# Performance work log

Hardware: AMD Instinct MI355X
Metric: run time of the kernel (lower is better)

## Reference

```python
import jax, jax.numpy as jnp
import numpy as np

H = 1024      # hidden_size
NH = 16       # num_attention_heads
DK = H // NH  # head dim
C = 1024      # cyclic_size


def setup_inputs() -> dict:
    key = jax.random.key(0)
    ks = jax.random.split(key, 13)
    B, S = 2, 2048
    s = 1.0 / np.sqrt(H)
    inp = {
        "q": jax.random.normal(ks[0], (B, S, H), jnp.float32),
        "k": jax.random.normal(ks[1], (B, S, H), jnp.float32),
        "v": jax.random.normal(ks[2], (B, S, H), jnp.float32),
        "Wq": jax.random.normal(ks[3], (H, H), jnp.float32) * s,
        "bq": jnp.zeros((H,), jnp.float32),
        "Wk": jax.random.normal(ks[4], (H, H), jnp.float32) * s,
        "bk": jnp.zeros((H,), jnp.float32),
        "Wv": jax.random.normal(ks[5], (H, H), jnp.float32) * s,
        "bv": jnp.zeros((H,), jnp.float32),
        "Wo": jax.random.normal(ks[6], (H, H), jnp.float32) * s,
        "bo": jnp.zeros((H,), jnp.float32),
        "Wc": jax.random.normal(ks[7], (H, C), jnp.float32) * s,
        "bc": jnp.zeros((C,), jnp.float32),
    }
    return inp


def _split_heads(x):
    B, S, _ = x.shape
    return x.reshape(B, S, NH, DK).transpose(0, 2, 1, 3)  # [B,NH,S,DK]


def reference(q, k, v, Wq, bq, Wk, bk, Wv, bv, Wo, bo, Wc, bc):
    Q = _split_heads(q @ Wq + bq)
    K = _split_heads(k @ Wk + bk)
    V = _split_heads(v @ Wv + bv)
    # unfused SDPA: full [B,NH,S,S] scores, as in the original module
    scores = jnp.einsum("bhqd,bhkd->bhqk", Q, K) / jnp.sqrt(jnp.float32(DK))
    probs = jax.nn.softmax(scores, axis=-1)
    attn = jnp.einsum("bhqk,bhkd->bhqd", probs, V)  # [B,NH,S,DK]
    B, _, S, _ = attn.shape
    merged = attn.transpose(0, 2, 1, 3).reshape(B, S, H)
    h = merged @ Wo + bo
    c = merged @ Wc + bc
    return (c, h)
```

## Files before the change

### kernel.cpp

```cpp
#include <hip/hip_runtime.h>
#include <stdint.h>

typedef unsigned short u16;
typedef short bf16x8 __attribute__((ext_vector_type(8)));
typedef short bf16x4 __attribute__((ext_vector_type(4)));
typedef float f32x4 __attribute__((ext_vector_type(4)));

#define MB (1u<<20)
#define CL2 0.18033688f

static __device__ __forceinline__ u16 f2bf(float x){
  union { float f; unsigned u; } v; v.f = x;
  return (u16)((v.u + 0x7FFFu + ((v.u >> 16) & 1u)) >> 16);
}

static __device__ __forceinline__ void gld_lds16(const void* g, void* l){
  __builtin_amdgcn_global_load_lds((const __attribute__((address_space(1))) unsigned int*)g,
                                   (__attribute__((address_space(3))) unsigned int*)l, 16, 0, 0);
}

static __device__ __forceinline__ int pack_bf16(float a, float b){
  unsigned ua = __float_as_uint(a) + 0x8000u;
  unsigned ub = __float_as_uint(b) + 0x8000u;
  return (int)__builtin_amdgcn_perm(ub, ua, 0x07060302u);
}

__global__ void convx(const float* __restrict__ q, const float* __restrict__ k, const float* __restrict__ v,
                      u16* __restrict__ qb, u16* __restrict__ kb, u16* __restrict__ vb){
  const float* s = blockIdx.z==0 ? q : (blockIdx.z==1 ? k : v);
  u16* d = blockIdx.z==0 ? qb : (blockIdx.z==1 ? kb : vb);
  int i = (blockIdx.x*256 + threadIdx.x)*4;
  float4 f = *(const float4*)(s + i);
  ushort4 o; o.x=f2bf(f.x); o.y=f2bf(f.y); o.z=f2bf(f.z); o.w=f2bf(f.w);
  *(ushort4*)(d + i) = o;
}

__global__ void convw(const float* W0,const float* W1,const float* W2,const float* W3,const float* W4,
                      u16* T0,u16* T1,u16* T2,u16* T3,u16* T4){
  const float* W = blockIdx.z==0?W0:blockIdx.z==1?W1:blockIdx.z==2?W2:blockIdx.z==3?W3:W4;
  u16* T = blockIdx.z==0?T0:blockIdx.z==1?T1:blockIdx.z==2?T2:blockIdx.z==3?T3:T4;
  __shared__ u16 t[64][65];
  int k0 = blockIdx.x*64, n0 = blockIdx.y*64;
  for (int i=0;i<16;i++){
    int idx = i*256 + threadIdx.x;
    int r = idx >> 6, c = idx & 63;
    t[r][c] = f2bf(W[(size_t)(k0+r)*1024 + n0 + c]);
  }
  __syncthreads();
  for (int i=0;i<2;i++){
    int idx = i*256 + threadIdx.x;
    int nl = idx >> 3, kc = idx & 7;
    bf16x8 o;
    #pragma unroll
    for (int j=0;j<8;j++) o[j] = (short)t[kc*8+j][nl];
    *(bf16x8*)(T + (size_t)(n0+nl)*1024 + k0 + kc*8) = o;
  }
}

template<int MODE>
static __device__ __forceinline__ void gemm_bt_dev(u16* __restrict__ As, u16* __restrict__ Bs,
                                                   const u16* __restrict__ A, const u16* __restrict__ Bt,
                                                   const float* __restrict__ bias, void* __restrict__ Cout){
  const int tid = threadIdx.x, lane = tid & 63, w = tid >> 6;
  const int wm = w >> 1, wn = w & 1, quad = lane >> 4, lr = lane & 15;
  const int fid = blockIdx.y * 8 + blockIdx.x;
  const int o   = (fid & 7) * 32 + (fid >> 3);
  const int n0  = (o & 7) * 128, m0 = (o >> 3) * 128;
  f32x4 acc[4][4] = {};
  const u16* Ab = A + (size_t)m0*1024;
  const u16* Bb = Bt + (size_t)n0*1024;
  const int srow_base = w*8 + (lane >> 3);
  const int sg = lane & 7;
  for (int k0 = 0; k0 < 1024; k0 += 64){
    #pragma unroll
    for (int j = 0; j < 4; ++j){
      int row = j*32 + srow_base;
      int g = sg ^ (row & 7);
      gld_lds16(Ab + (size_t)row*1024 + k0 + g*8, As + (j*32 + w*8)*64);
      gld_lds16(Bb + (size_t)row*1024 + k0 + g*8, Bs + (j*32 + w*8)*64);
    }
    __syncthreads();
    #pragma unroll
    for (int kk = 0; kk < 2; ++kk){
      bf16x8 af[4], bfr[4];
      #pragma unroll
      for (int i=0;i<4;i++){
        int ra = wm*64 + i*16 + lr;
        af[i]  = *(const bf16x8*)(As + ra*64 + (((kk*4+quad) ^ (ra & 7)))*8);
        int rb = wn*64 + i*16 + lr;
        bfr[i] = *(const bf16x8*)(Bs + rb*64 + (((kk*4+quad) ^ (rb & 7)))*8);
      }
      #pragma unroll
      for (int mi=0;mi<4;mi++)
        #pragma unroll
        for (int ni=0;ni<4;ni++)
          acc[mi][ni] = __builtin_amdgcn_mfma_f32_16x16x32_bf16(af[mi], bfr[ni], acc[mi][ni], 0, 0, 0);
    }
    __syncthreads();
  }
  #pragma unroll
  for (int mi=0;mi<4;mi++){
    int row = m0 + wm*64 + mi*16 + quad*4;
    #pragma unroll
    for (int ni=0;ni<4;ni++){
      int col = n0 + wn*64 + ni*16 + lr;
      float bb = bias[col];
      #pragma unroll
      for (int rg=0; rg<4; rg++){
        float vv = acc[mi][ni][rg] + bb;
        int r = row + rg;
        if (MODE == 0){
          ((u16*)Cout)[(size_t)r*1024 + col] = f2bf(vv);
        } else if (MODE == 4){
          ((u16*)Cout)[(size_t)r*1024 + col] = f2bf(vv * CL2);
        } else if (MODE == 1){
          ((float*)Cout)[(size_t)r*1024 + col] = vv;
        } else if (MODE == 2){
          int b2 = r >> 11, s = r & 2047, kb2 = s >> 7, kvl = s & 127;
          int hh = col >> 6, hg = (col & 63) >> 3, hl = col & 7;
          ((u16*)Cout)[((size_t)(b2*16+hh)*16 + kb2)*8192 + hg*1024 + kvl*8 + hl] = f2bf(vv);
        } else {
          int b2 = r >> 11, s = r & 2047, kb2 = s >> 7, kvl = s & 127;
          int mt2v = kvl >> 5, gv = (kvl >> 2) & 3, jv = ((kvl >> 4) & 1)*4 + (kvl & 3);
          int hh = col >> 6, dd = col & 63;
          ((u16*)Cout)[((size_t)(b2*16+hh)*16 + kb2)*8192 + (size_t)(mt2v*4+gv)*512 + dd*8 + jv] = f2bf(vv);
        }
      }
    }
  }
}

__global__ void qkv_gemm(const u16* qb,const u16* kb,const u16* vb,
                         const u16* Wqt,const u16* Wkt,const u16* Wvt,
                         const float* bq,const float* bk,const float* bv,
                         u16* Qb,u16* Kr,u16* Vr){
  __shared__ u16 As[128*64];
  __shared__ u16 Bs[128*64];
  if (blockIdx.z == 0)      gemm_bt_dev<4>(As, Bs, qb, Wqt, bq, Qb);
  else if (blockIdx.z == 1) gemm_bt_dev<2>(As, Bs, kb, Wkt, bk, Kr);
  else                      gemm_bt_dev<3>(As, Bs, vb, Wvt, bv, Vr);
}

__global__ void out_gemm(const u16* Mg, const u16* Wct, const u16* Wot,
                         const float* bc, const float* bo, float* out){
  __shared__ u16 As[128*64];
  __shared__ u16 Bs[128*64];
  const u16* B = blockIdx.z==0? Wct : Wot;
  const float* bias = blockIdx.z==0? bc : bo;
  float* C = out + (blockIdx.z==0? 0 : 4194304);
  gemm_bt_dev<1>(As, Bs, Mg, B, bias, C);
}

__global__ __launch_bounds__(256,2) void attn(const u16* __restrict__ Qb, const u16* __restrict__ Kr,
                                              const u16* __restrict__ Vr, u16* __restrict__ Mg){
  __shared__ u16 Ks[2][8192];
  __shared__ u16 Vs[2][8192];
  const int fid = blockIdx.y * 16 + blockIdx.x;
  const int o   = (fid & 7) * 64 + (fid >> 3);
  const int qt = o & 15, bh = o >> 4, b = bh >> 4, h = bh & 15;
  const int tid = threadIdx.x, lane = tid & 63, w = tid >> 6;
  const int quad = lane >> 4, lr = lane & 15;
  const int q0 = qt*128 + w*32;

  bf16x8 aq[2][2];
  #pragma unroll
  for (int t=0;t<2;t++)
    #pragma unroll
    for (int ks=0;ks<2;ks++)
      aq[t][ks] = *(const bf16x8*)(Qb + (size_t)(b*2048 + q0 + t*16 + lr)*1024 + h*64 + ks*32 + quad*8);

  f32x4 acco[2][4] = {};
  f32x4 accl[2] = {};
  const bf16x8 ones8 = {(short)0x3F80,(short)0x3F80,(short)0x3F80,(short)0x3F80,
                        (short)0x3F80,(short)0x3F80,(short)0x3F80,(short)0x3F80};

  const u16* Krb = Kr + (size_t)bh*131072;
  const u16* Vrb = Vr + (size_t)bh*131072;

  #pragma unroll
  for (int j=0;j<4;j++){
    gld_lds16(Krb + j*2048 + tid*8, &Ks[0][j*2048 + w*512]);
    gld_lds16(Vrb + j*2048 + tid*8, &Vs[0][j*2048 + w*512]);
  }

  for (int kb = 0; kb < 16; kb++){
    __syncthreads();
    const int cur = kb & 1;
    if (kb < 15){
      const u16* kg = Krb + (size_t)(kb+1)*8192;
      const u16* vg = Vrb + (size_t)(kb+1)*8192;
      #pragma unroll
      for (int j=0;j<4;j++){
        gld_lds16(kg + j*2048 + tid*8, &Ks[cur^1][j*2048 + w*512]);
        gld_lds16(vg + j*2048 + tid*8, &Vs[cur^1][j*2048 + w*512]);
      }
    }
    const u16* Ksc = Ks[cur];
    const u16* Vsc = Vs[cur];

    #pragma unroll
    for (int mt2=0;mt2<4;mt2++){
      f32x4 ae0 = {}, ae1 = {}, ao0 = {}, ao1 = {};
      {
        bf16x8 kf0 = *(const bf16x8*)(Ksc + (0*4+quad)*1024 + ((2*mt2)*16+lr)*8);
        bf16x8 kf1 = *(const bf16x8*)(Ksc + (1*4+quad)*1024 + ((2*mt2)*16+lr)*8);
        ae0 = __builtin_amdgcn_mfma_f32_16x16x32_bf16(kf0, aq[0][0], ae0, 0,0,0);
        ae1 = __builtin_amdgcn_mfma_f32_16x16x32_bf16(kf0, aq[1][0], ae1, 0,0,0);
        ae0 = __builtin_amdgcn_mfma_f32_16x16x32_bf16(kf1, aq[0][1], ae0, 0,0,0);
        ae1 = __builtin_amdgcn_mfma_f32_16x16x32_bf16(kf1, aq[1][1], ae1, 0,0,0);
      }
      {
        bf16x8 kf0 = *(const bf16x8*)(Ksc + (0*4+quad)*1024 + ((2*mt2+1)*16+lr)*8);
        bf16x8 kf1 = *(const bf16x8*)(Ksc + (1*4+quad)*1024 + ((2*mt2+1)*16+lr)*8);
        ao0 = __builtin_amdgcn_mfma_f32_16x16x32_bf16(kf0, aq[0][0], ao0, 0,0,0);
        ao1 = __builtin_amdgcn_mfma_f32_16x16x32_bf16(kf0, aq[1][0], ao1, 0,0,0);
        ao0 = __builtin_amdgcn_mfma_f32_16x16x32_bf16(kf1, aq[0][1], ao0, 0,0,0);
        ao1 = __builtin_amdgcn_mfma_f32_16x16x32_bf16(kf1, aq[1][1], ao1, 0,0,0);
      }

      union { int4 i4; bf16x8 v; } pf0, pf1;
      pf0.i4.x = pack_bf16(__builtin_amdgcn_exp2f(ae0[0]), __builtin_amdgcn_exp2f(ae0[1]));
      pf0.i4.y = pack_bf16(__builtin_amdgcn_exp2f(ae0[2]), __builtin_amdgcn_exp2f(ae0[3]));
      pf0.i4.z = pack_bf16(__builtin_amdgcn_exp2f(ao0[0]), __builtin_amdgcn_exp2f(ao0[1]));
      pf0.i4.w = pack_bf16(__builtin_amdgcn_exp2f(ao0[2]), __builtin_amdgcn_exp2f(ao0[3]));
      pf1.i4.x = pack_bf16(__builtin_amdgcn_exp2f(ae1[0]), __builtin_amdgcn_exp2f(ae1[1]));
      pf1.i4.y = pack_bf16(__builtin_amdgcn_exp2f(ae1[2]), __builtin_amdgcn_exp2f(ae1[3]));
      pf1.i4.z = pack_bf16(__builtin_amdgcn_exp2f(ao1[0]), __builtin_amdgcn_exp2f(ao1[1]));
      pf1.i4.w = pack_bf16(__builtin_amdgcn_exp2f(ao1[2]), __builtin_amdgcn_exp2f(ao1[3]));

      accl[0] = __builtin_amdgcn_mfma_f32_16x16x32_bf16(ones8, pf0.v, accl[0], 0,0,0);
      accl[1] = __builtin_amdgcn_mfma_f32_16x16x32_bf16(ones8, pf1.v, accl[1], 0,0,0);

      #pragma unroll
      for (int dt=0;dt<4;dt++){
        bf16x8 vf = *(const bf16x8*)(Vsc + (mt2*4+quad)*512 + (dt*16+lr)*8);
        acco[0][dt] = __builtin_amdgcn_mfma_f32_16x16x32_bf16(vf, pf0.v, acco[0][dt], 0,0,0);
        acco[1][dt] = __builtin_amdgcn_mfma_f32_16x16x32_bf16(vf, pf1.v, acco[1][dt], 0,0,0);
      }
    }
  }

  #pragma unroll
  for (int t=0;t<2;t++){
    float inv = 1.f / accl[t][0];
    u16* dst = Mg + (size_t)(b*2048 + q0 + t*16 + lr)*1024 + h*64;
    #pragma unroll
    for (int dt=0;dt<4;dt++){
      bf16x4 o2;
      #pragma unroll
      for (int rg=0;rg<4;rg++) o2[rg] = (short)f2bf(acco[t][dt][rg]*inv);
      *(bf16x4*)(dst + dt*16 + quad*4) = o2;
    }
  }
}

extern "C" void kernel_launch(void* const* d_in, const int* in_sizes, int n_in,
                              void* d_out, int out_size, void* d_ws, size_t ws_size,
                              hipStream_t stream){
  const float* q  = (const float*)d_in[0];
  const float* k  = (const float*)d_in[1];
  const float* v  = (const float*)d_in[2];
  const float* Wq = (const float*)d_in[3];
  const float* bq = (const float*)d_in[4];
  const float* Wk = (const float*)d_in[5];
  const float* bk = (const float*)d_in[6];
  const float* Wv = (const float*)d_in[7];
  const float* bv = (const float*)d_in[8];
  const float* Wo = (const float*)d_in[9];
  const float* bo = (const float*)d_in[10];
  const float* Wc = (const float*)d_in[11];
  const float* bc = (const float*)d_in[12];
  char* ws = (char*)d_ws;
  u16* qb  = (u16*)(ws + (size_t)0*MB);
  u16* kb  = (u16*)(ws + (size_t)8*MB);
  u16* vb  = (u16*)(ws + (size_t)16*MB);
  u16* Wqt = (u16*)(ws + (size_t)24*MB);
  u16* Wkt = (u16*)(ws + (size_t)26*MB);
  u16* Wvt = (u16*)(ws + (size_t)28*MB);
  u16* Wot = (u16*)(ws + (size_t)30*MB);
  u16* Wct = (u16*)(ws + (size_t)32*MB);
  u16* Qb  = (u16*)(ws + (size_t)34*MB);
  u16* Kr  = (u16*)(ws + (size_t)42*MB);
  u16* Vr  = (u16*)(ws + (size_t)50*MB);
  u16* Mg  = (u16*)(ws + (size_t)58*MB);

  dim3 blk(256,1,1);
  hipLaunchKernelGGL(convx,    dim3(4096,1,3), blk, 0, stream, q,k,v, qb,kb,vb);
  hipLaunchKernelGGL(convw,    dim3(16,16,5),  blk, 0, stream, Wq,Wk,Wv,Wo,Wc, Wqt,Wkt,Wvt,Wot,Wct);
  hipLaunchKernelGGL(qkv_gemm, dim3(8,32,3),   blk, 0, stream, qb,kb,vb, Wqt,Wkt,Wvt, bq,bk,bv, Qb,Kr,Vr);
  hipLaunchKernelGGL(attn,     dim3(16,32,1),  blk, 0, stream, Qb, Kr, Vr, Mg);
  hipLaunchKernelGGL(out_gemm, dim3(8,32,2),   blk, 0, stream, Mg, Wct, Wot, bc, bo, (float*)d_out);
}
```

Measured before the change: 226.7 us.

## Split attention over KV halves with separate combine kernel

Splits each attention block's key/value range into two halves along a new grid dimension, with smaller 64-key LDS stages and a higher occupancy launch bound. Each half writes a normalized partial output and its row sum, and a new combine kernel merges them with weights proportional to the row sums. This doubles the number of attention blocks to fill more CUs and raises waves per CU, at the cost of an extra kernel launch and extra global traffic for the partial outputs. The partial outputs are stored as bf16, which adds a second rounding step.

```diff
diff --git a/kernel.cpp b/kernel.cpp
--- a/kernel.cpp
+++ b/kernel.cpp
@@ -12,6 +12,11 @@
 static __device__ __forceinline__ u16 f2bf(float x){
   union { float f; unsigned u; } v; v.f = x;
   return (u16)((v.u + 0x7FFFu + ((v.u >> 16) & 1u)) >> 16);
+}
+
+static __device__ __forceinline__ float bf2f(u16 x){
+  union { unsigned u; float f; } v; v.u = ((unsigned)x) << 16;
+  return v.f;
 }
 
 static __device__ __forceinline__ void gld_lds16(const void* g, void* l){
@@ -151,13 +156,15 @@
   gemm_bt_dev<1>(As, Bs, Mg, B, bias, C);
 }
 
-__global__ __launch_bounds__(256,2) void attn(const u16* __restrict__ Qb, const u16* __restrict__ Kr,
-                                              const u16* __restrict__ Vr, u16* __restrict__ Mg){
-  __shared__ u16 Ks[2][8192];
-  __shared__ u16 Vs[2][8192];
+__global__ __launch_bounds__(256,4) void attn(const u16* __restrict__ Qb, const u16* __restrict__ Kr,
+                                              const u16* __restrict__ Vr, u16* __restrict__ Opart,
+                                              float* __restrict__ lpart){
+  __shared__ u16 Ks[2][4096];
+  __shared__ u16 Vs[2][4096];
   const int fid = blockIdx.y * 16 + blockIdx.x;
   const int o   = (fid & 7) * 64 + (fid >> 3);
   const int qt = o & 15, bh = o >> 4, b = bh >> 4, h = bh & 15;
+  const int kvh = blockIdx.z;
   const int tid = threadIdx.x, lane = tid & 63, w = tid >> 6;
   const int quad = lane >> 4, lr = lane & 15;
   const int q0 = qt*128 + w*32;
@@ -177,41 +184,40 @@
   const u16* Krb = Kr + (size_t)bh*131072;
   const u16* Vrb = Vr + (size_t)bh*131072;
 
-  #pragma unroll
-  for (int j=0;j<4;j++){
-    gld_lds16(Krb + j*2048 + tid*8, &Ks[0][j*2048 + w*512]);
-    gld_lds16(Vrb + j*2048 + tid*8, &Vs[0][j*2048 + w*512]);
-  }
-
-  for (int kb = 0; kb < 16; kb++){
+  #define STAGE_KV(t_, buf_) do{                                                  \
+    int kb2_ = (t_) >> 1, half_ = (t_) & 1;                                       \
+    const u16* kg_ = Krb + (size_t)kb2_*8192 + half_*512;                         \
+    const u16* vg_ = Vrb + (size_t)kb2_*8192 + half_*4096;                        \
+    _Pragma("unroll")                                                             \
+    for (int i_=0;i_<2;i_++){                                                     \
+      gld_lds16(kg_ + (i_*4+w)*1024 + lane*8, &Ks[buf_][i_*2048 + w*512]);        \
+      gld_lds16(vg_ + (i_*256 + w*64 + lane)*8, &Vs[buf_][i_*2048 + w*512]);      \
+    }                                                                             \
+  }while(0)
+
+  STAGE_KV(kvh*16, 0);
+
+  for (int it = 0; it < 16; it++){
     __syncthreads();
-    const int cur = kb & 1;
-    if (kb < 15){
-      const u16* kg = Krb + (size_t)(kb+1)*8192;
-      const u16* vg = Vrb + (size_t)(kb+1)*8192;
-      #pragma unroll
-      for (int j=0;j<4;j++){
-        gld_lds16(kg + j*2048 + tid*8, &Ks[cur^1][j*2048 + w*512]);
-        gld_lds16(vg + j*2048 + tid*8, &Vs[cur^1][j*2048 + w*512]);
-      }
-    }
+    const int cur = it & 1;
+    if (it < 15) STAGE_KV(kvh*16 + it + 1, cur^1);
     const u16* Ksc = Ks[cur];
     const u16* Vsc = Vs[cur];
 
     #pragma unroll
-    for (int mt2=0;mt2<4;mt2++){
+    for (int mt2=0;mt2<2;mt2++){
       f32x4 ae0 = {}, ae1 = {}, ao0 = {}, ao1 = {};
       {
-        bf16x8 kf0 = *(const bf16x8*)(Ksc + (0*4+quad)*1024 + ((2*mt2)*16+lr)*8);
-        bf16x8 kf1 = *(const bf16x8*)(Ksc + (1*4+quad)*1024 + ((2*mt2)*16+lr)*8);
+        bf16x8 kf0 = *(const bf16x8*)(Ksc + (0*4+quad)*512 + ((2*mt2)*16+lr)*8);
+        bf16x8 kf1 = *(const bf16x8*)(Ksc + (1*4+quad)*512 + ((2*mt2)*16+lr)*8);
         ae0 = __builtin_amdgcn_mfma_f32_16x16x32_bf16(kf0, aq[0][0], ae0, 0,0,0);
         ae1 = __builtin_amdgcn_mfma_f32_16x16x32_bf16(kf0, aq[1][0], ae1, 0,0,0);
         ae0 = __builtin_amdgcn_mfma_f32_16x16x32_bf16(kf1, aq[0][1], ae0, 0,0,0);
         ae1 = __builtin_amdgcn_mfma_f32_16x16x32_bf16(kf1, aq[1][1], ae1, 0,0,0);
       }
       {
-        bf16x8 kf0 = *(const bf16x8*)(Ksc + (0*4+quad)*1024 + ((2*mt2+1)*16+lr)*8);
-        bf16x8 kf1 = *(const bf16x8*)(Ksc + (1*4+quad)*1024 + ((2*mt2+1)*16+lr)*8);
+        bf16x8 kf0 = *(const bf16x8*)(Ksc + (0*4+quad)*512 + ((2*mt2+1)*16+lr)*8);
+        bf16x8 kf1 = *(const bf16x8*)(Ksc + (1*4+quad)*512 + ((2*mt2+1)*16+lr)*8);
         ao0 = __builtin_amdgcn_mfma_f32_16x16x32_bf16(kf0, aq[0][0], ao0, 0,0,0);
         ao1 = __builtin_amdgcn_mfma_f32_16x16x32_bf16(kf0, aq[1][0], ao1, 0,0,0);
         ao0 = __builtin_amdgcn_mfma_f32_16x16x32_bf16(kf1, aq[0][1], ao0, 0,0,0);
@@ -239,11 +245,16 @@
       }
     }
   }
-
+  #undef STAGE_KV
+
+  u16* Oh = Opart + (size_t)kvh*4194304;
+  float* lh = lpart + (size_t)kvh*65536;
   #pragma unroll
   for (int t=0;t<2;t++){
-    float inv = 1.f / accl[t][0];
-    u16* dst = Mg + (size_t)(b*2048 + q0 + t*16 + lr)*1024 + h*64;
+    int r = b*2048 + q0 + t*16 + lr;
+    float lv = accl[t][0];
+    float inv = 1.f / lv;
+    u16* dst = Oh + (size_t)r*1024 + h*64;
     #pragma unroll
     for (int dt=0;dt<4;dt++){
       bf16x4 o2;
@@ -251,7 +262,22 @@
       for (int rg=0;rg<4;rg++) o2[rg] = (short)f2bf(acco[t][dt][rg]*inv);
       *(bf16x4*)(dst + dt*16 + quad*4) = o2;
     }
-  }
+    if (quad == 0) lh[r*16 + h] = lv;
+  }
+}
+
+__global__ void attn_combine(const u16* __restrict__ Opart, const float* __restrict__ lpart,
+                             u16* __restrict__ Mg){
+  int r = blockIdx.x, c = threadIdx.x*4, h = threadIdx.x >> 4;
+  float l0 = lpart[r*16 + h], l1 = lpart[65536 + r*16 + h];
+  float w0 = l0 / (l0 + l1), w1 = 1.f - w0;
+  bf16x4 x = *(const bf16x4*)(Opart + (size_t)r*1024 + c);
+  bf16x4 y = *(const bf16x4*)(Opart + 4194304 + (size_t)r*1024 + c);
+  bf16x4 o2;
+  #pragma unroll
+  for (int rg=0;rg<4;rg++)
+    o2[rg] = (short)f2bf(w0*bf2f((u16)x[rg]) + w1*bf2f((u16)y[rg]));
+  *(bf16x4*)(Mg + (size_t)r*1024 + c) = o2;
 }
 
 extern "C" void kernel_launch(void* const* d_in, const int* in_sizes, int n_in,
@@ -283,11 +309,14 @@
   u16* Kr  = (u16*)(ws + (size_t)42*MB);
   u16* Vr  = (u16*)(ws + (size_t)50*MB);
   u16* Mg  = (u16*)(ws + (size_t)58*MB);
+  u16*  Opart = (u16*)(ws + (size_t)0*MB);
+  float* lpart = (float*)(ws + (size_t)16*MB);
 
   dim3 blk(256,1,1);
   hipLaunchKernelGGL(convx,    dim3(4096,1,3), blk, 0, stream, q,k,v, qb,kb,vb);
   hipLaunchKernelGGL(convw,    dim3(16,16,5),  blk, 0, stream, Wq,Wk,Wv,Wo,Wc, Wqt,Wkt,Wvt,Wot,Wct);
   hipLaunchKernelGGL(qkv_gemm, dim3(8,32,3),   blk, 0, stream, qb,kb,vb, Wqt,Wkt,Wvt, bq,bk,bv, Qb,Kr,Vr);
-  hipLaunchKernelGGL(attn,     dim3(16,32,1),  blk, 0, stream, Qb, Kr, Vr, Mg);
+  hipLaunchKernelGGL(attn,     dim3(16,32,2),  blk, 0, stream, Qb, Kr, Vr, Opart, lpart);
+  hipLaunchKernelGGL(attn_combine, dim3(4096,1,1), blk, 0, stream, Opart, lpart, Mg);
   hipLaunchKernelGGL(out_gemm, dim3(8,32,2),   blk, 0, stream, Mg, Wct, Wot, bc, bo, (float*)d_out);
 }
```

After: 238.3 us. +5.1%, slower.

## Fuse fp32-to-bf16 input conversion into QKV GEMM, add MFMA priority hints

Applied to the files above, without the earlier changes.

Removes the separate convx kernel. The QKV GEMM now reads fp32 activations directly, converts them to bf16 in registers and stores them swizzled into LDS, prefetching the next K-tile into registers while the current one is consumed. This saves one launch plus a full write and re-read of the bf16 activations. The cost is that the A operand no longer uses async LDS loads and the fp32 reads double that operand's traffic inside the GEMM. The attention loop also raises wave priority around its MFMA sections with s_setprio, to favour matrix-core issue over the exp/pack work of other waves.

```diff
diff --git a/kernel.cpp b/kernel.cpp
--- a/kernel.cpp
+++ b/kernel.cpp
@@ -23,16 +23,6 @@
   unsigned ua = __float_as_uint(a) + 0x8000u;
   unsigned ub = __float_as_uint(b) + 0x8000u;
   return (int)__builtin_amdgcn_perm(ub, ua, 0x07060302u);
-}
-
-__global__ void convx(const float* __restrict__ q, const float* __restrict__ k, const float* __restrict__ v,
-                      u16* __restrict__ qb, u16* __restrict__ kb, u16* __restrict__ vb){
-  const float* s = blockIdx.z==0 ? q : (blockIdx.z==1 ? k : v);
-  u16* d = blockIdx.z==0 ? qb : (blockIdx.z==1 ? kb : vb);
-  int i = (blockIdx.x*256 + threadIdx.x)*4;
-  float4 f = *(const float4*)(s + i);
-  ushort4 o; o.x=f2bf(f.x); o.y=f2bf(f.y); o.z=f2bf(f.z); o.w=f2bf(f.w);
-  *(ushort4*)(d + i) = o;
 }
 
 __global__ void convw(const float* W0,const float* W1,const float* W2,const float* W3,const float* W4,
@@ -57,9 +47,9 @@
   }
 }
 
-template<int MODE>
+template<int MODE, bool AF32>
 static __device__ __forceinline__ void gemm_bt_dev(u16* __restrict__ As, u16* __restrict__ Bs,
-                                                   const u16* __restrict__ A, const u16* __restrict__ Bt,
+                                                   const void* __restrict__ Av, const u16* __restrict__ Bt,
                                                    const float* __restrict__ bias, void* __restrict__ Cout){
   const int tid = threadIdx.x, lane = tid & 63, w = tid >> 6;
   const int wm = w >> 1, wn = w & 1, quad = lane >> 4, lr = lane & 15;
@@ -67,19 +57,50 @@
   const int o   = (fid & 7) * 32 + (fid >> 3);
   const int n0  = (o & 7) * 128, m0 = (o >> 3) * 128;
   f32x4 acc[4][4] = {};
-  const u16* Ab = A + (size_t)m0*1024;
-  const u16* Bb = Bt + (size_t)n0*1024;
+  const float* Af = (const float*)Av + (size_t)m0*1024;
+  const u16*   Ab = (const u16*)Av + (size_t)m0*1024;
+  const u16*   Bb = Bt + (size_t)n0*1024;
   const int srow_base = w*8 + (lane >> 3);
   const int sg = lane & 7;
-  for (int k0 = 0; k0 < 1024; k0 += 64){
-    #pragma unroll
-    for (int j = 0; j < 4; ++j){
+
+  bf16x8 areg[4];
+  auto LOADA = [&](int kn){
+    #pragma unroll
+    for (int j=0;j<4;++j){
       int row = j*32 + srow_base;
       int g = sg ^ (row & 7);
-      gld_lds16(Ab + (size_t)row*1024 + k0 + g*8, As + (j*32 + w*8)*64);
-      gld_lds16(Bb + (size_t)row*1024 + k0 + g*8, Bs + (j*32 + w*8)*64);
-    }
-    __syncthreads();
+      const float* ap = Af + (size_t)row*1024 + kn + g*8;
+      float4 f0 = *(const float4*)ap;
+      float4 f1 = *(const float4*)(ap+4);
+      bf16x8 r;
+      r[0]=(short)f2bf(f0.x); r[1]=(short)f2bf(f0.y); r[2]=(short)f2bf(f0.z); r[3]=(short)f2bf(f0.w);
+      r[4]=(short)f2bf(f1.x); r[5]=(short)f2bf(f1.y); r[6]=(short)f2bf(f1.z); r[7]=(short)f2bf(f1.w);
+      areg[j] = r;
+    }
+  };
+  if constexpr (AF32) LOADA(0);
+
+  for (int k0 = 0; k0 < 1024; k0 += 64){
+    if constexpr (AF32){
+      #pragma unroll
+      for (int j = 0; j < 4; ++j){
+        int row = j*32 + srow_base;
+        *(bf16x8*)(As + row*64 + sg*8) = areg[j];
+        int g = sg ^ (row & 7);
+        gld_lds16(Bb + (size_t)row*1024 + k0 + g*8, Bs + (j*32 + w*8)*64);
+      }
+      __syncthreads();
+      if (k0 < 960) LOADA(k0 + 64);
+    } else {
+      #pragma unroll
+      for (int j = 0; j < 4; ++j){
+        int row = j*32 + srow_base;
+        int g = sg ^ (row & 7);
+        gld_lds16(Ab + (size_t)row*1024 + k0 + g*8, As + (j*32 + w*8)*64);
+        gld_lds16(Bb + (size_t)row*1024 + k0 + g*8, Bs + (j*32 + w*8)*64);
+      }
+      __syncthreads();
+    }
     #pragma unroll
     for (int kk = 0; kk < 2; ++kk){
       bf16x8 af[4], bfr[4];
@@ -130,15 +151,15 @@
   }
 }
 
-__global__ void qkv_gemm(const u16* qb,const u16* kb,const u16* vb,
+__global__ void qkv_gemm(const float* q,const float* k,const float* v,
                          const u16* Wqt,const u16* Wkt,const u16* Wvt,
                          const float* bq,const float* bk,const float* bv,
                          u16* Qb,u16* Kr,u16* Vr){
   __shared__ u16 As[128*64];
   __shared__ u16 Bs[128*64];
-  if (blockIdx.z == 0)      gemm_bt_dev<4>(As, Bs, qb, Wqt, bq, Qb);
-  else if (blockIdx.z == 1) gemm_bt_dev<2>(As, Bs, kb, Wkt, bk, Kr);
-  else                      gemm_bt_dev<3>(As, Bs, vb, Wvt, bv, Vr);
+  if (blockIdx.z == 0)      gemm_bt_dev<4,true>(As, Bs, q, Wqt, bq, Qb);
+  else if (blockIdx.z == 1) gemm_bt_dev<2,true>(As, Bs, k, Wkt, bk, Kr);
+  else                      gemm_bt_dev<3,true>(As, Bs, v, Wvt, bv, Vr);
 }
 
 __global__ void out_gemm(const u16* Mg, const u16* Wct, const u16* Wot,
@@ -148,7 +169,7 @@
   const u16* B = blockIdx.z==0? Wct : Wot;
   const float* bias = blockIdx.z==0? bc : bo;
   float* C = out + (blockIdx.z==0? 0 : 4194304);
-  gemm_bt_dev<1>(As, Bs, Mg, B, bias, C);
+  gemm_bt_dev<1,false>(As, Bs, Mg, B, bias, C);
 }
 
 __global__ __launch_bounds__(256,2) void attn(const u16* __restrict__ Qb, const u16* __restrict__ Kr,
@@ -201,6 +222,7 @@
     #pragma unroll
     for (int mt2=0;mt2<4;mt2++){
       f32x4 ae0 = {}, ae1 = {}, ao0 = {}, ao1 = {};
+      __builtin_amdgcn_s_setprio(1);
       {
         bf16x8 kf0 = *(const bf16x8*)(Ksc + (0*4+quad)*1024 + ((2*mt2)*16+lr)*8);
         bf16x8 kf1 = *(const bf16x8*)(Ksc + (1*4+quad)*1024 + ((2*mt2)*16+lr)*8);
@@ -217,6 +239,7 @@
         ao0 = __builtin_amdgcn_mfma_f32_16x16x32_bf16(kf1, aq[0][1], ao0, 0,0,0);
         ao1 = __builtin_amdgcn_mfma_f32_16x16x32_bf16(kf1, aq[1][1], ao1, 0,0,0);
       }
+      __builtin_amdgcn_s_setprio(0);
 
       union { int4 i4; bf16x8 v; } pf0, pf1;
       pf0.i4.x = pack_bf16(__builtin_amdgcn_exp2f(ae0[0]), __builtin_amdgcn_exp2f(ae0[1]));
@@ -228,6 +251,7 @@
       pf1.i4.z = pack_bf16(__builtin_amdgcn_exp2f(ao1[0]), __builtin_amdgcn_exp2f(ao1[1]));
       pf1.i4.w = pack_bf16(__builtin_amdgcn_exp2f(ao1[2]), __builtin_amdgcn_exp2f(ao1[3]));
 
+      __builtin_amdgcn_s_setprio(1);
       accl[0] = __builtin_amdgcn_mfma_f32_16x16x32_bf16(ones8, pf0.v, accl[0], 0,0,0);
       accl[1] = __builtin_amdgcn_mfma_f32_16x16x32_bf16(ones8, pf1.v, accl[1], 0,0,0);
 
@@ -237,6 +261,7 @@
         acco[0][dt] = __builtin_amdgcn_mfma_f32_16x16x32_bf16(vf, pf0.v, acco[0][dt], 0,0,0);
         acco[1][dt] = __builtin_amdgcn_mfma_f32_16x16x32_bf16(vf, pf1.v, acco[1][dt], 0,0,0);
       }
+      __builtin_amdgcn_s_setprio(0);
     }
   }
 
@@ -271,9 +296,6 @@
   const float* Wc = (const float*)d_in[11];
   const float* bc = (const float*)d_in[12];
   char* ws = (char*)d_ws;
-  u16* qb  = (u16*)(ws + (size_t)0*MB);
-  u16* kb  = (u16*)(ws + (size_t)8*MB);
-  u16* vb  = (u16*)(ws + (size_t)16*MB);
   u16* Wqt = (u16*)(ws + (size_t)24*MB);
   u16* Wkt = (u16*)(ws + (size_t)26*MB);
   u16* Wvt = (u16*)(ws + (size_t)28*MB);
@@ -285,9 +307,8 @@
   u16* Mg  = (u16*)(ws + (size_t)58*MB);
 
   dim3 blk(256,1,1);
-  hipLaunchKernelGGL(convx,    dim3(4096,1,3), blk, 0, stream, q,k,v, qb,kb,vb);
   hipLaunchKernelGGL(convw,    dim3(16,16,5),  blk, 0, stream, Wq,Wk,Wv,Wo,Wc, Wqt,Wkt,Wvt,Wot,Wct);
-  hipLaunchKernelGGL(qkv_gemm, dim3(8,32,3),   blk, 0, stream, qb,kb,vb, Wqt,Wkt,Wvt, bq,bk,bv, Qb,Kr,Vr);
+  hipLaunchKernelGGL(qkv_gemm, dim3(8,32,3),   blk, 0, stream, q,k,v, Wqt,Wkt,Wvt, bq,bk,bv, Qb,Kr,Vr);
   hipLaunchKernelGGL(attn,     dim3(16,32,1),  blk, 0, stream, Qb, Kr, Vr, Mg);
   hipLaunchKernelGGL(out_gemm, dim3(8,32,2),   blk, 0, stream, Mg, Wct, Wot, bc, bo, (float*)d_out);
 }
```

New measurement: 244.6 us. +7.9%, slower.
